# Optimization experiments

Hardware: AMD Instinct MI355X
Metric: run time of the kernel (lower is better)

Reference implementation:

```python
import jax, jax.numpy as jnp
import numpy as np
import math

DIM, HEADS, WS, RED = 192, 6, 7, 4
HD = DIM // HEADS
N = WS * WS
BW = 4096  # total windows (B_)


def _pdsca(x, ca_w1, ca_b1, ca_w2, ca_b2, sa_w, sa_b):
    # Parallel dual channel+spatial attention producing mask logits, same shape as x.
    # x: (B, C, 7, 7)
    ca = x.mean(axis=(2, 3))                              # (B, C) global avg pool
    h = jax.nn.gelu(ca @ ca_w1.T + ca_b1)                 # (B, C/r)
    ca = h @ ca_w2.T + ca_b2                              # (B, C)
    sa_in = jnp.concatenate([x.mean(axis=1, keepdims=True),
                             x.max(axis=1, keepdims=True)], axis=1)  # (B, 2, 7, 7)
    sa = jax.lax.conv_general_dilated(sa_in, sa_w, (1, 1), 'SAME',
                                      dimension_numbers=('NCHW', 'OIHW', 'NCHW'))
    sa = sa + sa_b[None, :, None, None]                   # (B, 1, 7, 7)
    return ca[:, :, None, None] + sa                      # broadcast to (B, C, 7, 7)


def _forward(qkv, log_temp, pos_w, pos_b, pos_scale,
             meta_w1, meta_b1, meta_w2, meta_b2,
             q_ca_w1, q_ca_b1, q_ca_w2, q_ca_b2, q_sa_w, q_sa_b,
             k_ca_w1, k_ca_b1, k_ca_w2, k_ca_b2, k_sa_w, k_sa_b,
             proj_w):
    B = qkv.shape[0]
    qkv5 = qkv.reshape(B, N, 3, HEADS, HD).transpose(2, 0, 3, 1, 4)  # (3, B, H, N, hd)
    q, k, v = qkv5[0], qkv5[1], qkv5[2]

    temperature = jnp.exp(log_temp)

    # sigmoid gates on q and k via PDSCA on (B*H, hd, 7, 7) windows
    mq = _pdsca(q.reshape(-1, HD, WS, WS), q_ca_w1, q_ca_b1, q_ca_w2, q_ca_b2, q_sa_w, q_sa_b)
    mk = _pdsca(k.reshape(-1, HD, WS, WS), k_ca_w1, k_ca_b1, k_ca_w2, k_ca_b2, k_sa_w, k_sa_b)
    q = q * jax.nn.sigmoid(mq.reshape(q.shape))
    k = k * jax.nn.sigmoid(mk.reshape(k.shape))

    attn = jnp.einsum('bhnd,bhmd->bhnm', q, k) * temperature  # (B, H, N, N)

    # learned relative position bias: conv1x1 on coord grid -> pairwise diffs -> meta MLP
    coords = jnp.linspace(-1.0, 1.0, WS)
    yg, xg = jnp.meshgrid(coords, coords, indexing='ij')
    grid = jnp.stack([xg, yg], axis=0)                        # (2, 7, 7)
    pe = jnp.einsum('chw,dc->dhw', grid, pos_w) + pos_b[:, None, None]  # (dim, 7, 7)
    pef = pe.reshape(DIM, N).T                                # (N, dim)
    rel = pos_scale * (pef[:, None, :] - pef[None, :, :])     # (N, N, dim)
    bias = jax.nn.gelu(rel @ meta_w1 + meta_b1) @ meta_w2 + meta_b2  # (N, N, H)
    bias = bias.transpose(2, 0, 1)                            # (H, N, N)

    attn = jax.nn.softmax(attn + bias[None], axis=-1)
    out = jnp.einsum('bhnm,bhmd->bnhd', attn, v).reshape(B, N, DIM)
    return out @ proj_w.T                                     # project_out 1x1 conv


def setup_inputs() -> dict:
    key = jax.random.key(0)
    ks = jax.random.split(key, 24)
    s = 0.02
    d = {
        'qkv': jax.random.normal(ks[0], (BW, N, 3 * DIM), dtype=jnp.float32),
        'log_temp': jnp.array([math.log(0.1)], dtype=jnp.float32),
        'pos_w': jax.random.normal(ks[1], (DIM, 2), dtype=jnp.float32) * s,
        'pos_b': jnp.zeros((DIM,), dtype=jnp.float32),
        'pos_scale': jnp.float32(0.1),
        'meta_w1': jax.random.normal(ks[2], (DIM, 128), dtype=jnp.float32) * s,
        'meta_b1': jnp.zeros((128,), dtype=jnp.float32),
        'meta_w2': jax.random.normal(ks[3], (128, HEADS), dtype=jnp.float32) * s,
        'meta_b2': jnp.zeros((HEADS,), dtype=jnp.float32),
        'q_ca_w1': jax.random.normal(ks[4], (HD // RED, HD), dtype=jnp.float32) * s,
        'q_ca_b1': jnp.zeros((HD // RED,), dtype=jnp.float32),
        'q_ca_w2': jax.random.normal(ks[5], (HD, HD // RED), dtype=jnp.float32) * s,
        'q_ca_b2': jnp.zeros((HD,), dtype=jnp.float32),
        'q_sa_w': jax.random.normal(ks[6], (1, 2, 7, 7), dtype=jnp.float32) * s,
        'q_sa_b': jnp.zeros((1,), dtype=jnp.float32),
        'k_ca_w1': jax.random.normal(ks[7], (HD // RED, HD), dtype=jnp.float32) * s,
        'k_ca_b1': jnp.zeros((HD // RED,), dtype=jnp.float32),
        'k_ca_w2': jax.random.normal(ks[8], (HD, HD // RED), dtype=jnp.float32) * s,
        'k_ca_b2': jnp.zeros((HD,), dtype=jnp.float32),
        'k_sa_w': jax.random.normal(ks[9], (1, 2, 7, 7), dtype=jnp.float32) * s,
        'k_sa_b': jnp.zeros((1,), dtype=jnp.float32),
        'proj_w': jax.random.normal(ks[10], (DIM, DIM), dtype=jnp.float32) * s,
    }
    return d


def reference(qkv, log_temp, pos_w, pos_b, pos_scale,
              meta_w1, meta_b1, meta_w2, meta_b2,
              q_ca_w1, q_ca_b1, q_ca_w2, q_ca_b2, q_sa_w, q_sa_b,
              k_ca_w1, k_ca_b1, k_ca_w2, k_ca_b2, k_sa_w, k_sa_b,
              proj_w):
    return _forward(qkv, log_temp, pos_w, pos_b, pos_scale,
                    meta_w1, meta_b1, meta_w2, meta_b2,
                    q_ca_w1, q_ca_b1, q_ca_w2, q_ca_b2, q_sa_w, q_sa_b,
                    k_ca_w1, k_ca_b1, k_ca_w2, k_ca_b2, k_sa_w, k_sa_b,
                    proj_w)
```

## Files before the change

### kernel.cpp

```cpp
#include <hip/hip_runtime.h>
#include <math.h>

#define DIM 192
#define HEADS 6
#define HD 32
#define WS 7
#define NN 49
#define NWIN 4096
#define QKV_ROW (3*DIM)

typedef __attribute__((ext_vector_type(8))) short bf16x8_t;
typedef __attribute__((ext_vector_type(4))) float f32x4_t;

#define MFMA16(a,b,c) __builtin_amdgcn_mfma_f32_16x16x32_bf16((a),(b),(c),0,0,0)

__device__ __forceinline__ float gelu_tanh(float x) {
    const float k0 = 0.7978845608028654f;
    const float k1 = 0.044715f;
    float t = tanhf(k0 * (x + k1 * x * x * x));
    return 0.5f * x * (1.0f + t);
}
__device__ __forceinline__ unsigned short f2bf(float f) {
    __bf16 h = (__bf16)f;
    return __builtin_bit_cast(unsigned short, h);
}
__device__ __forceinline__ float bf2f(unsigned short u) {
    return (float)__builtin_bit_cast(__bf16, u);
}

#define BIASF_FLOATS (HEADS*64*64)
#define WBF_OFF_B    (BIASF_FLOATS*4)

__global__ __launch_bounds__(128) void bias_kernel(
    const float* __restrict__ pos_w, const float* __restrict__ pos_scale,
    const float* __restrict__ meta_w1, const float* __restrict__ meta_b1,
    const float* __restrict__ meta_w2, const float* __restrict__ meta_b2,
    float* __restrict__ bias_frag)
{
    const int p = blockIdx.x;
    const int n = p / NN, m = p % NN;
    const int i = threadIdx.x;
    __shared__ float hbuf[128];
    const float step = 2.0f / 6.0f;
    const float dx = (float)((n % WS) - (m % WS)) * step;
    const float dy = (float)((n / WS) - (m / WS)) * step;
    const float ps = pos_scale[0];
    float a = meta_b1[i];
    for (int d = 0; d < DIM; ++d) {
        float rel = ps * (pos_w[2*d] * dx + pos_w[2*d+1] * dy);
        a += rel * meta_w1[d*128 + i];
    }
    hbuf[i] = gelu_tanh(a);
    __syncthreads();
    if (i < HEADS) {
        float b = meta_b2[i];
        for (int j = 0; j < 128; ++j) b += hbuf[j] * meta_w2[j*HEADS + i];
        bias_frag[((i*64 + n)*16 + (m & 15))*4 + (m >> 4)] = b;
    }
}

__global__ __launch_bounds__(256) void prep_w(
    const float* __restrict__ proj_w, unsigned short* __restrict__ wbf,
    float* __restrict__ bias_frag)
{
    int idx = blockIdx.x*256 + threadIdx.x;
    if (idx < DIM*DIM) wbf[idx] = f2bf(proj_w[idx]);
    int z = idx - DIM*DIM;
    if (z >= 0 && z < HEADS*15*64) {
        int hh = z / 960, rem = z - hh*960;
        int row = 49 + (rem >> 6), inner = rem & 63;
        bias_frag[(hh*64 + row)*64 + inner] = 0.f;
    }
}

#define QS  200
#define RSV 72

#define G_SM 0
#define G_MX 49
#define G_CA 98
#define G_SA 130

__device__ __forceinline__ void gate_one(
    unsigned short* xs, int hoff,
    const float* __restrict__ w1, const float* __restrict__ b1,
    const float* __restrict__ w2, const float* __restrict__ b2,
    const float* sw, float sab, float* scr, int l)
{
    int c = l & 31, h2 = l >> 5;
    int s0 = h2 ? 25 : 0, s1 = h2 ? 49 : 25;
    float s = 0.f;
    for (int sp = s0; sp < s1; ++sp) {
        int j = c*NN + sp;
        s += bf2f(xs[(j >> 5)*QS + hoff + (j & 31)]);
    }
    s += __shfl_xor(s, 32);
    float cm = s * (1.f/49.f);
    int o = l & 7, t8 = l >> 3;
    float part = 0.f;
    #pragma unroll
    for (int kk = 0; kk < 4; ++kk) {
        int c2 = t8 + (kk << 3);
        part += w1[(o << 5) + c2] * __shfl(cm, c2);
    }
    part += __shfl_xor(part, 8);
    part += __shfl_xor(part, 16);
    part += __shfl_xor(part, 32);
    float hid = gelu_tanh(part + b1[o]);
    float a2 = b2[c];
    #pragma unroll
    for (int oo = 0; oo < 8; ++oo)
        a2 += w2[(c << 3) + oo] * __shfl(hid, oo);
    scr[G_CA + c] = a2;
    if (l < NN) {
        float sm = 0.f, mx = -1e30f;
        #pragma unroll
        for (int c2 = 0; c2 < HD; ++c2) {
            int j2 = c2*NN + l;
            float v = bf2f(xs[(j2 >> 5)*QS + hoff + (j2 & 31)]);
            sm += v; mx = fmaxf(mx, v);
        }
        scr[G_SM + l] = sm * (1.f/HD);
        scr[G_MX + l] = mx;
        int y = l / WS, x = l - y*WS;
        int y0 = max(0, y-3), y1 = min(6, y+3);
        int x0 = max(0, x-3), x1 = min(6, x+3);
        float a = sab;
        for (int iy = y0; iy <= y1; ++iy) {
            int ky = iy - y + 3;
            for (int ix = x0; ix <= x1; ++ix) {
                int kx = ix - x + 3;
                int s2 = iy*WS + ix;
                a += sw[ky*WS+kx] * scr[G_SM+s2] + sw[NN+ky*WS+kx] * scr[G_MX+s2];
            }
        }
        scr[G_SA + l] = a;
    }
    for (int j = l; j < NN*HD; j += 64) {
        int c2 = j / NN, sp = j - c2*NN;
        int idx = (j >> 5)*QS + hoff + (j & 31);
        float g = 1.f / (1.f + __expf(-(scr[G_CA+c2] + scr[G_SA+sp])));
        xs[idx] = f2bf(bf2f(xs[idx]) * g);
    }
}

__global__ __launch_bounds__(384) void win_attn_mfma(
    const float* __restrict__ qkv,
    const float* __restrict__ log_temp,
    const float* __restrict__ q_ca_w1, const float* __restrict__ q_ca_b1,
    const float* __restrict__ q_ca_w2, const float* __restrict__ q_ca_b2,
    const float* __restrict__ q_sa_w, const float* __restrict__ q_sa_b,
    const float* __restrict__ k_ca_w1, const float* __restrict__ k_ca_b1,
    const float* __restrict__ k_ca_w2, const float* __restrict__ k_ca_b2,
    const float* __restrict__ k_sa_w, const float* __restrict__ k_sa_b,
    const float* __restrict__ bias_frag,
    const unsigned short* __restrict__ wbf,
    float* __restrict__ out)
{
    __shared__ __align__(16) unsigned short q_all[NN*QS];
    __shared__ __align__(16) unsigned short k_all[NN*QS];
    __shared__ __align__(16) unsigned short p_all[HEADS][16*RSV];
    __shared__ __align__(16) float sw_s[196];

    const int t = threadIdx.x;
    const int b = blockIdx.x;
    const int w = t >> 6;
    const int l = t & 63;
    const int lrow = l & 15;
    const int lk = l >> 4;
    const int lk8 = lk * 8;
    const int hoff = w * HD;
    unsigned short* p_w = p_all[w];
    float* scr = (float*)p_w;
    const float temp = __expf(log_temp[0]);
    const float* qkv_b = qkv + (size_t)b * (NN*QKV_ROW);

    for (int i = l; i < 196; i += 64)
        sw_s[i] = (i < 98) ? q_sa_w[i] : k_sa_w[i-98];

    bf16x8_t vfrag[2][2];
    #pragma unroll
    for (int ks = 0; ks < 2; ++ks)
        #pragma unroll
        for (int nt = 0; nt < 2; ++nt) {
            bf16x8_t f;
            #pragma unroll
            for (int e = 0; e < 8; ++e) {
                int m = ks*32 + lk8 + e;
                float v = 0.f;
                if (m < NN)
                    v = qkv_b[(size_t)m*QKV_ROW + 2*DIM + hoff + nt*16 + lrow];
                f[e] = (short)f2bf(v);
            }
            vfrag[ks][nt] = f;
        }

    for (int e = l; e < NN*8; e += 64) {
        int n = e >> 3, c = e & 7;
        const float* base = qkv_b + n*QKV_ROW + hoff + (c<<2);
        float4 fq = *(const float4*)(base);
        float4 fk = *(const float4*)(base + DIM);
        ushort4 uq = { f2bf(fq.x), f2bf(fq.y), f2bf(fq.z), f2bf(fq.w) };
        ushort4 uk = { f2bf(fk.x), f2bf(fk.y), f2bf(fk.z), f2bf(fk.w) };
        *(ushort4*)&q_all[n*QS + hoff + (c<<2)] = uq;
        *(ushort4*)&k_all[n*QS + hoff + (c<<2)] = uk;
    }

    gate_one(q_all, hoff, q_ca_w1, q_ca_b1, q_ca_w2, q_ca_b2, sw_s,      q_sa_b[0], scr, l);
    gate_one(k_all, hoff, k_ca_w1, k_ca_b1, k_ca_w2, k_ca_b2, sw_s + 98, k_sa_b[0], scr, l);

    const float* bias_f = bias_frag + w*64*64;
    #pragma unroll 1
    for (int s = 0; s < 4; ++s) {
        int ar = s*16 + lrow;
        int ac = ar < NN ? ar : NN-1;
        bf16x8_t aq = *(const bf16x8_t*)&q_all[ac*QS + hoff + lk8];
        f32x4_t sac[4];
        #pragma unroll
        for (int j = 0; j < 4; ++j) {
            int mr = j*16 + lrow;
            int mc = mr < NN ? mr : NN-1;
            bf16x8_t bk = *(const bf16x8_t*)&k_all[mc*QS + hoff + lk8];
            f32x4_t z = (f32x4_t){0.f,0.f,0.f,0.f};
            sac[j] = MFMA16(aq, bk, z);
        }
        #pragma unroll
        for (int r = 0; r < 4; ++r) {
            int row = s*16 + lk*4 + r;
            float4 b4 = *(const float4*)(bias_f + (row*16 + lrow)*4);
            float v0 = sac[0][r]*temp + b4.x;
            float v1 = sac[1][r]*temp + b4.y;
            float v2 = sac[2][r]*temp + b4.z;
            float v3 = (lrow == 0) ? (sac[3][r]*temp + b4.w) : -1e30f;
            float mx = fmaxf(fmaxf(v0, v1), fmaxf(v2, v3));
            mx = fmaxf(mx, __shfl_xor(mx, 1));
            mx = fmaxf(mx, __shfl_xor(mx, 2));
            mx = fmaxf(mx, __shfl_xor(mx, 4));
            mx = fmaxf(mx, __shfl_xor(mx, 8));
            float e0 = __expf(v0 - mx), e1 = __expf(v1 - mx);
            float e2 = __expf(v2 - mx), e3 = __expf(v3 - mx);
            float sum = e0 + e1 + e2 + e3;
            sum += __shfl_xor(sum, 1);
            sum += __shfl_xor(sum, 2);
            sum += __shfl_xor(sum, 4);
            sum += __shfl_xor(sum, 8);
            float inv = 1.f / sum;
            int pb = (lk*4 + r)*RSV + lrow;
            p_w[pb +  0] = f2bf(e0 * inv);
            p_w[pb + 16] = f2bf(e1 * inv);
            p_w[pb + 32] = f2bf(e2 * inv);
            p_w[pb + 48] = f2bf(e3 * inv);
        }
        f32x4_t oac[2];
        oac[0] = (f32x4_t){0.f,0.f,0.f,0.f};
        oac[1] = (f32x4_t){0.f,0.f,0.f,0.f};
        #pragma unroll
        for (int ks = 0; ks < 2; ++ks) {
            bf16x8_t ap = *(const bf16x8_t*)&p_w[lrow*RSV + ks*32 + lk8];
            #pragma unroll
            for (int nt = 0; nt < 2; ++nt)
                oac[nt] = MFMA16(ap, vfrag[ks][nt], oac[nt]);
        }
        #pragma unroll
        for (int nt = 0; nt < 2; ++nt)
            #pragma unroll
            for (int r = 0; r < 4; ++r) {
                int row = s*16 + lk*4 + r;
                if (row < NN)
                    q_all[row*QS + hoff + nt*16 + lrow] = f2bf(oac[nt][r]);
            }
    }

    __syncthreads();

    f32x4_t pacc[4][2];
    #pragma unroll
    for (int s2 = 0; s2 < 4; ++s2) {
        pacc[s2][0] = (f32x4_t){0.f,0.f,0.f,0.f};
        pacc[s2][1] = (f32x4_t){0.f,0.f,0.f,0.f};
    }
    #pragma unroll
    for (int s2 = 0; s2 < 4; ++s2) {
        int ar = s2*16 + lrow;
        int ac = ar < NN ? ar : NN-1;
        #pragma unroll
        for (int c = 0; c < 6; ++c) {
            bf16x8_t ao = *(const bf16x8_t*)&q_all[ac*QS + c*32 + lk8];
            #pragma unroll
            for (int jj = 0; jj < 2; ++jj) {
                bf16x8_t bw = *(const bf16x8_t*)(wbf + ((2*w+jj)*16 + lrow)*DIM + c*32 + lk8);
                pacc[s2][jj] = MFMA16(ao, bw, pacc[s2][jj]);
            }
        }
    }
    float* out_b = out + (size_t)b * (NN*DIM);
    #pragma unroll
    for (int s2 = 0; s2 < 4; ++s2)
        #pragma unroll
        for (int jj = 0; jj < 2; ++jj)
            #pragma unroll
            for (int r = 0; r < 4; ++r) {
                int row = s2*16 + lk*4 + r;
                if (row < NN)
                    out_b[row*DIM + (2*w+jj)*16 + lrow] = pacc[s2][jj][r];
            }
}

extern "C" void kernel_launch(void* const* d_in, const int* in_sizes, int n_in,
                              void* d_out, int out_size, void* d_ws, size_t ws_size,
                              hipStream_t stream)
{
    (void)in_sizes; (void)n_in; (void)out_size; (void)ws_size;
    const float* qkv      = (const float*)d_in[0];
    const float* log_temp = (const float*)d_in[1];
    const float* pos_w    = (const float*)d_in[2];
    const float* pos_scale= (const float*)d_in[4];
    const float* meta_w1  = (const float*)d_in[5];
    const float* meta_b1  = (const float*)d_in[6];
    const float* meta_w2  = (const float*)d_in[7];
    const float* meta_b2  = (const float*)d_in[8];
    const float* q_ca_w1  = (const float*)d_in[9];
    const float* q_ca_b1  = (const float*)d_in[10];
    const float* q_ca_w2  = (const float*)d_in[11];
    const float* q_ca_b2  = (const float*)d_in[12];
    const float* q_sa_w   = (const float*)d_in[13];
    const float* q_sa_b   = (const float*)d_in[14];
    const float* k_ca_w1  = (const float*)d_in[15];
    const float* k_ca_b1  = (const float*)d_in[16];
    const float* k_ca_w2  = (const float*)d_in[17];
    const float* k_ca_b2  = (const float*)d_in[18];
    const float* k_sa_w   = (const float*)d_in[19];
    const float* k_sa_b   = (const float*)d_in[20];
    const float* proj_w   = (const float*)d_in[21];
    float* out = (float*)d_out;

    float* bias_frag = (float*)d_ws;
    unsigned short* wbf = (unsigned short*)((char*)d_ws + WBF_OFF_B);

    hipLaunchKernelGGL(bias_kernel, dim3(NN*NN), dim3(128), 0, stream,
                       pos_w, pos_scale, meta_w1, meta_b1, meta_w2, meta_b2, bias_frag);
    hipLaunchKernelGGL(prep_w, dim3((DIM*DIM + HEADS*15*64 + 255)/256), dim3(256), 0, stream,
                       proj_w, wbf, bias_frag);
    hipLaunchKernelGGL(win_attn_mfma, dim3(NWIN), dim3(384), 0, stream,
                       qkv, log_temp,
                       q_ca_w1, q_ca_b1, q_ca_w2, q_ca_b2, q_sa_w, q_sa_b,
                       k_ca_w1, k_ca_b1, k_ca_w2, k_ca_b2, k_sa_w, k_sa_b,
                       bias_frag, wbf, out);
}
```

Baseline: 398.4 us.

## Share one LDS buffer for q and k, gating fragments in registers

Merges the separate q and k shared-memory tiles into one buffer. K values are held in registers while q is staged, gated and loaded into MFMA fragments, then k overwrites the same buffer. The sigmoid gate is now applied while building fragments in registers instead of being written back to LDS, and the score loop is fully unrolled over preloaded q/k fragments. Halving LDS use should let more blocks share a CU, but it raises VGPR pressure (7 float4 k values plus 8 fragments) and recomputes some gate values redundantly.

```diff
diff --git a/kernel.cpp b/kernel.cpp
--- a/kernel.cpp
+++ b/kernel.cpp
@@ -81,8 +81,8 @@
 #define G_CA 98
 #define G_SA 130
 
-__device__ __forceinline__ void gate_one(
-    unsigned short* xs, int hoff,
+__device__ __forceinline__ void stats_one(
+    const unsigned short* xs, int hoff,
     const float* __restrict__ w1, const float* __restrict__ b1,
     const float* __restrict__ w2, const float* __restrict__ b2,
     const float* sw, float sab, float* scr, int l)
@@ -136,12 +136,22 @@
         }
         scr[G_SA + l] = a;
     }
-    for (int j = l; j < NN*HD; j += 64) {
-        int c2 = j / NN, sp = j - c2*NN;
-        int idx = (j >> 5)*QS + hoff + (j & 31);
-        float g = 1.f / (1.f + __expf(-(scr[G_CA+c2] + scr[G_SA+sp])));
-        xs[idx] = f2bf(bf2f(xs[idx]) * g);
-    }
+}
+
+__device__ __forceinline__ bf16x8_t gate_frag(
+    const unsigned short* xs, int hoff, int row, int lk8, const float* scr)
+{
+    bf16x8_t r = *(const bf16x8_t*)&xs[row*QS + hoff + lk8];
+    bf16x8_t g;
+    int flat = row*HD + lk8;
+    #pragma unroll
+    for (int e = 0; e < 8; ++e) {
+        int f = flat + e;
+        int c = f / NN, sp = f - c*NN;
+        float gg = 1.f / (1.f + __expf(-(scr[G_CA+c] + scr[G_SA+sp])));
+        g[e] = (short)f2bf(bf2f((unsigned short)r[e]) * gg);
+    }
+    return g;
 }
 
 __global__ __launch_bounds__(384) void win_attn_mfma(
@@ -157,8 +167,7 @@
     const unsigned short* __restrict__ wbf,
     float* __restrict__ out)
 {
-    __shared__ __align__(16) unsigned short q_all[NN*QS];
-    __shared__ __align__(16) unsigned short k_all[NN*QS];
+    __shared__ __align__(16) unsigned short x_all[NN*QS];
     __shared__ __align__(16) unsigned short p_all[HEADS][16*RSV];
     __shared__ __align__(16) float sw_s[196];
 
@@ -195,34 +204,54 @@
             vfrag[ks][nt] = f;
         }
 
-    for (int e = l; e < NN*8; e += 64) {
-        int n = e >> 3, c = e & 7;
-        const float* base = qkv_b + n*QKV_ROW + hoff + (c<<2);
-        float4 fq = *(const float4*)(base);
-        float4 fk = *(const float4*)(base + DIM);
-        ushort4 uq = { f2bf(fq.x), f2bf(fq.y), f2bf(fq.z), f2bf(fq.w) };
-        ushort4 uk = { f2bf(fk.x), f2bf(fk.y), f2bf(fk.z), f2bf(fk.w) };
-        *(ushort4*)&q_all[n*QS + hoff + (c<<2)] = uq;
-        *(ushort4*)&k_all[n*QS + hoff + (c<<2)] = uk;
-    }
-
-    gate_one(q_all, hoff, q_ca_w1, q_ca_b1, q_ca_w2, q_ca_b2, sw_s,      q_sa_b[0], scr, l);
-    gate_one(k_all, hoff, k_ca_w1, k_ca_b1, k_ca_w2, k_ca_b2, sw_s + 98, k_sa_b[0], scr, l);
-
-    const float* bias_f = bias_frag + w*64*64;
-    #pragma unroll 1
+    float4 kr[7];
+    #pragma unroll
+    for (int i = 0; i < 7; ++i) {
+        int e = l + i*64;
+        if (e < NN*8) {
+            int n = e >> 3, c = e & 7;
+            const float* base = qkv_b + n*QKV_ROW + hoff + (c<<2);
+            float4 fq = *(const float4*)(base);
+            kr[i] = *(const float4*)(base + DIM);
+            ushort4 uq = { f2bf(fq.x), f2bf(fq.y), f2bf(fq.z), f2bf(fq.w) };
+            *(ushort4*)&x_all[n*QS + hoff + (c<<2)] = uq;
+        }
+    }
+
+    stats_one(x_all, hoff, q_ca_w1, q_ca_b1, q_ca_w2, q_ca_b2, sw_s, q_sa_b[0], scr, l);
+    bf16x8_t qfrag[4];
+    #pragma unroll
     for (int s = 0; s < 4; ++s) {
         int ar = s*16 + lrow;
-        int ac = ar < NN ? ar : NN-1;
-        bf16x8_t aq = *(const bf16x8_t*)&q_all[ac*QS + hoff + lk8];
+        qfrag[s] = gate_frag(x_all, hoff, ar < NN ? ar : NN-1, lk8, scr);
+    }
+
+    #pragma unroll
+    for (int i = 0; i < 7; ++i) {
+        int e = l + i*64;
+        if (e < NN*8) {
+            int n = e >> 3, c = e & 7;
+            ushort4 uk = { f2bf(kr[i].x), f2bf(kr[i].y), f2bf(kr[i].z), f2bf(kr[i].w) };
+            *(ushort4*)&x_all[n*QS + hoff + (c<<2)] = uk;
+        }
+    }
+
+    stats_one(x_all, hoff, k_ca_w1, k_ca_b1, k_ca_w2, k_ca_b2, sw_s + 98, k_sa_b[0], scr, l);
+    bf16x8_t kfrag[4];
+    #pragma unroll
+    for (int j = 0; j < 4; ++j) {
+        int mr = j*16 + lrow;
+        kfrag[j] = gate_frag(x_all, hoff, mr < NN ? mr : NN-1, lk8, scr);
+    }
+
+    const float* bias_f = bias_frag + w*64*64;
+    #pragma unroll
+    for (int s = 0; s < 4; ++s) {
         f32x4_t sac[4];
         #pragma unroll
         for (int j = 0; j < 4; ++j) {
-            int mr = j*16 + lrow;
-            int mc = mr < NN ? mr : NN-1;
-            bf16x8_t bk = *(const bf16x8_t*)&k_all[mc*QS + hoff + lk8];
             f32x4_t z = (f32x4_t){0.f,0.f,0.f,0.f};
-            sac[j] = MFMA16(aq, bk, z);
+            sac[j] = MFMA16(qfrag[s], kfrag[j], z);
         }
         #pragma unroll
         for (int r = 0; r < 4; ++r) {
@@ -267,7 +296,7 @@
             for (int r = 0; r < 4; ++r) {
                 int row = s*16 + lk*4 + r;
                 if (row < NN)
-                    q_all[row*QS + hoff + nt*16 + lrow] = f2bf(oac[nt][r]);
+                    x_all[row*QS + hoff + nt*16 + lrow] = f2bf(oac[nt][r]);
             }
     }
 
@@ -285,7 +314,7 @@
         int ac = ar < NN ? ar : NN-1;
         #pragma unroll
         for (int c = 0; c < 6; ++c) {
-            bf16x8_t ao = *(const bf16x8_t*)&q_all[ac*QS + c*32 + lk8];
+            bf16x8_t ao = *(const bf16x8_t*)&x_all[ac*QS + c*32 + lk8];
             #pragma unroll
             for (int jj = 0; jj < 2; ++jj) {
                 bf16x8_t bw = *(const bf16x8_t*)(wbf + ((2*w+jj)*16 + lrow)*DIM + c*32 + lk8);
```

Result: slower. 599.9 us (+50.6%).
